# Performance work log

Hardware: AMD Instinct MI355X
Metric: run time of the kernel (lower is better)

The kernel has to match this reference:

```python
import jax, jax.numpy as jnp
import numpy as np

B, N, D, H = 8, 2048, 128, 8
HD = D // H  # head_depth = 16
CLIP = 10.0
INF = 1e10
THETA = 10000.0
SCALE_BASE = 512.0
LOGIT_SCALE = float(np.log(400.0) / np.log(50.0) / np.sqrt(HD))


def _rotate_half(x):
    # interleaved pairs: (x1, x2) -> (-x2, x1)
    x1 = x[..., ::2]
    x2 = x[..., 1::2]
    return jnp.stack((-x2, x1), axis=-1).reshape(x.shape)


def _rope_xpos(n, hd):
    # rotary_embedding_torch RotaryEmbedding(dim=hd, use_xpos=True)
    inv_freq = 1.0 / (THETA ** (jnp.arange(0, hd, 2, dtype=jnp.float32) / hd))  # (hd/2,)
    t = jnp.arange(n, dtype=jnp.float32)
    freqs = t[:, None] * inv_freq[None, :]          # (n, hd/2)
    freqs = jnp.repeat(freqs, 2, axis=-1)           # (n, hd) interleaved dup
    sc = (jnp.arange(0, hd, 2, dtype=jnp.float32) + 0.4 * hd) / (1.4 * hd)  # (hd/2,)
    power = (t - (n // 2)) / SCALE_BASE             # centered positions
    scale = sc[None, :] ** power[:, None]           # (n, hd/2)
    scale = jnp.repeat(scale, 2, axis=-1)           # (n, hd)
    return freqs, scale


def setup_inputs() -> dict:
    key = jax.random.key(0)
    ks = jax.random.split(key, 7)
    stdv_qkv = 1.0 / np.sqrt(HD)
    stdv_out = 1.0 / np.sqrt(D)
    q = jax.random.normal(ks[0], (B, N, D), dtype=jnp.float32)
    k = jax.random.normal(ks[1], (B, N, D), dtype=jnp.float32)
    v = jax.random.normal(ks[2], (B, N, D), dtype=jnp.float32)
    Wq = jax.random.uniform(ks[3], (D, D), minval=-stdv_qkv, maxval=stdv_qkv, dtype=jnp.float32)
    Wk = jax.random.uniform(ks[4], (D, D), minval=-stdv_qkv, maxval=stdv_qkv, dtype=jnp.float32)
    Wv = jax.random.uniform(ks[5], (D, D), minval=-stdv_qkv, maxval=stdv_qkv, dtype=jnp.float32)
    Wout = jax.random.uniform(ks[6], (D, D), minval=-stdv_out, maxval=stdv_out, dtype=jnp.float32)
    mask = jnp.zeros((B, N, 1), dtype=bool)
    return {"q": q, "k": k, "v": v, "Wq": Wq, "Wk": Wk, "Wv": Wv, "Wout": Wout, "mask": mask}


def reference(q, k, v, Wq, Wk, Wv, Wout, mask):
    def split_heads(t, W):
        # torch Linear (bias=False): t @ W.T, then (B,N,H,HD) -> (B,H,N,HD)
        return (t @ W.T).reshape(B, N, H, HD).transpose(0, 2, 1, 3)

    Qh = split_heads(q, Wq)
    Kh = split_heads(k, Wk)
    Vh = split_heads(v, Wv)

    freqs, scale = _rope_xpos(N, HD)  # (N, HD) each, broadcast over (B,H,N,HD)
    cos, sin = jnp.cos(freqs), jnp.sin(freqs)
    Qr = Qh * (cos * scale) + _rotate_half(Qh) * (sin * scale)
    inv_scale = 1.0 / scale
    Kr = Kh * (cos * inv_scale) + _rotate_half(Kh) * (sin * inv_scale)

    logits = jnp.einsum('bhqd,bhkd->bhqk', Qr, Kr) * LOGIT_SCALE
    logits = CLIP * jnp.tanh(logits)
    # mask: (B,N,1) bool, True -> masked; broadcast to (B,1,1,N)
    logits = jnp.where(mask[:, None, None, :, 0], -INF, logits)
    probs = jax.nn.softmax(logits, axis=-1)
    out = jnp.einsum('bhqk,bhkd->bhqd', probs, Vh)
    out = out.transpose(0, 2, 1, 3).reshape(B, N, D)
    return out @ Wout.T
```

## Files before the change

### kernel.cpp

```cpp
#include <hip/hip_runtime.h>
#include <math.h>

#define BB 8
#define NN 2048
#define DD 128
#define HH 8

typedef _Float16 v4h __attribute__((ext_vector_type(4)));
typedef float    v4f __attribute__((ext_vector_type(4)));
struct h8 { v4h a, b; };

__device__ __forceinline__ v4f zero4() { v4f z = {0.f, 0.f, 0.f, 0.f}; return z; }

__device__ __forceinline__ v4f mfma16(v4h a, v4h b, v4f c) {
    return __builtin_amdgcn_mfma_f32_16x16x16f16(a, b, c, 0, 0, 0);
}

__device__ __forceinline__ float fexp2(float x) {
#if __has_builtin(__builtin_amdgcn_exp2f)
    return __builtin_amdgcn_exp2f(x);
#else
    return __expf(x * 0.69314718055994531f);
#endif
}

#define QSCALE 1.10478088f
#define C1F 14.426950408889634f
#define C2F 28.853900817779268f

__global__ __launch_bounds__(256) void prep_kernel(
    const float* __restrict__ Wq, const float* __restrict__ Wk,
    const float* __restrict__ Wv, const float* __restrict__ Wo,
    _Float16* __restrict__ WH, _Float16* __restrict__ WoH,
    float* __restrict__ rtab)
{
    int tid = blockIdx.x * 256 + threadIdx.x;
    int m = tid >> 14, i = tid & 16383;
    const float* src = (m == 0) ? Wq : (m == 1) ? Wk : (m == 2) ? Wv : Wo;
    float wv = src[i];
    if (m < 3) WH[m * 16384 + i] = (_Float16)wv;
    else       WoH[i] = (_Float16)wv;

    if (tid < NN * 16) {
        int t = tid >> 4, hd = tid & 15, j = hd >> 1;
        const float invf_tab[8] = {1.f, 0.31622776601683794f, 0.1f, 0.031622776601683791f,
                                   0.01f, 0.0031622776601683794f, 0.001f, 0.00031622776601683794f};
        float freq = (float)t * invf_tab[j];
        float c = cosf(freq), s = sinf(freq);
        float scf = ((float)(2 * j) + 6.4f) / 22.4f;
        float pw  = ((float)t - 1024.0f) / 512.0f;
        float scl = exp2f(pw * log2f(scf));
        rtab[0 * NN * 16 + tid] = c * scl * QSCALE;
        rtab[1 * NN * 16 + tid] = s * scl * QSCALE;
        float is = 1.0f / scl;
        rtab[2 * NN * 16 + tid] = c * is;
        rtab[3 * NN * 16 + tid] = s * is;
    }
}

__global__ __launch_bounds__(256) void proj_rope_kernel(
    const float* __restrict__ q, const float* __restrict__ k, const float* __restrict__ v,
    const _Float16* __restrict__ WH, const float* __restrict__ rtab,
    _Float16* __restrict__ Qr, _Float16* __restrict__ Kr, _Float16* __restrict__ VT)
{
    __shared__ __align__(16) _Float16 xb[64][136];
    const int tid = threadIdx.x;
    const int m  = blockIdx.y;
    const int r0 = blockIdx.x * 64;
    const int b  = r0 >> 11;
    const int n0 = r0 & 2047;

    const float* s = ((m == 0) ? q : (m == 1) ? k : v) + (size_t)r0 * 128;
    #pragma unroll
    for (int i = 0; i < 8; ++i) {
        int u = tid + i * 256;
        int row = u >> 5, c4 = (u & 31) * 4;
        v4f f = *(const v4f*)(s + row * 128 + c4);
        v4h hv; hv[0]=(_Float16)f[0]; hv[1]=(_Float16)f[1]; hv[2]=(_Float16)f[2]; hv[3]=(_Float16)f[3];
        *(v4h*)&xb[row][c4] = hv;
    }
    __syncthreads();

    const int w = tid >> 6, lane = tid & 63;
    const int l16 = lane & 15, quad = lane >> 4;

    v4h xf[8];
    #pragma unroll
    for (int kt = 0; kt < 8; ++kt)
        xf[kt] = *(const v4h*)&xb[w * 16 + l16][kt * 16 + quad * 4];
    const _Float16* Wm = WH + m * 16384;
    v4f acc[8];
    #pragma unroll
    for (int ct = 0; ct < 8; ++ct) acc[ct] = zero4();
    #pragma unroll
    for (int kt = 0; kt < 8; ++kt) {
        #pragma unroll
        for (int ct = 0; ct < 8; ++ct) {
            v4h wf = *(const v4h*)(Wm + (ct * 16 + l16) * 128 + kt * 16 + quad * 4);
            if (m < 2) acc[ct] = mfma16(wf, xf[kt], acc[ct]);
            else       acc[ct] = mfma16(xf[kt], wf, acc[ct]);
        }
    }
    if (m < 2) {
        const float* tc = rtab + (m == 0 ? 0 : 2 * NN * 16);
        const float* ts = tc + NN * 16;
        const int n = n0 + w * 16 + l16;
        _Float16* dst = (m == 0 ? Qr : Kr);
        #pragma unroll
        for (int ct = 0; ct < 8; ++ct) {
            v4f cs = *(const v4f*)(tc + n * 16 + quad * 4);
            v4f sn = *(const v4f*)(ts + n * 16 + quad * 4);
            v4f a = acc[ct];
            v4f rot; rot[0] = -a[1]; rot[1] = a[0]; rot[2] = -a[3]; rot[3] = a[2];
            v4h o;
            #pragma unroll
            for (int r = 0; r < 4; ++r) o[r] = (_Float16)(a[r] * cs[r] + rot[r] * sn[r]);
            *(v4h*)(dst + ((size_t)(b * 8 + ct) * NN + n) * 16 + quad * 4) = o;
        }
    } else {
        #pragma unroll
        for (int ct = 0; ct < 8; ++ct) {
            v4f a = acc[ct];
            v4h o;
            #pragma unroll
            for (int r = 0; r < 4; ++r) o[r] = (_Float16)a[r];
            *(v4h*)(VT + ((size_t)(b * 8 + ct) * 16 + l16) * NN + n0 + w * 16 + quad * 4) = o;
        }
    }
}

__global__ __launch_bounds__(64) void attn_kernel(
    const _Float16* __restrict__ Qr, const _Float16* __restrict__ Kr,
    const _Float16* __restrict__ VT, const unsigned char* __restrict__ mask,
    _Float16* __restrict__ Obuf)
{
    __shared__ __align__(16) _Float16 Kt[2][64][20];
    __shared__ __align__(16) _Float16 VTt[2][16][68];
    __shared__ __align__(16) float    av[2][64];

    const int tid = threadIdx.x;
    const int bh = blockIdx.x >> 6;
    const int qt = blockIdx.x & 63;
    const int b = bh >> 3, h = bh & 7;
    const int q0 = qt * 32;
    const int l16 = tid & 15, quad = tid >> 4;

    const _Float16* Kbase = Kr + (size_t)bh * NN * 16;
    const _Float16* Vbase = VT + (size_t)bh * 16 * NN;
    const unsigned char* mbase = mask + b * NN;

    v4h qf[2];
    #pragma unroll
    for (int g = 0; g < 2; ++g)
        qf[g] = *(const v4h*)(Qr + ((size_t)bh * NN + q0 + g * 16 + l16) * 16 + quad * 4);

    v4f ot[2], sa[2];
    #pragma unroll
    for (int g = 0; g < 2; ++g) { ot[g] = zero4(); sa[g] = zero4(); }
    v4h ones; ones[0] = ones[1] = ones[2] = ones[3] = (_Float16)1.f;

    const int vrow = tid >> 2, vcol = (tid & 3) * 16;

    {
        h8 kA = *(const h8*)(Kbase + (size_t)tid * 16);
        h8 kB = *(const h8*)(Kbase + (size_t)tid * 16 + 8);
        h8 vA = *(const h8*)(Vbase + (size_t)vrow * NN + vcol);
        h8 vB = *(const h8*)(Vbase + (size_t)vrow * NN + vcol + 8);
        float a0 = mbase[tid] ? -1e30f : C1F;
        *(v4h*)&Kt[0][tid][0]  = kA.a;  *(v4h*)&Kt[0][tid][4]  = kA.b;
        *(v4h*)&Kt[0][tid][8]  = kB.a;  *(v4h*)&Kt[0][tid][12] = kB.b;
        *(v4h*)&VTt[0][vrow][vcol]      = vA.a;  *(v4h*)&VTt[0][vrow][vcol + 4]  = vA.b;
        *(v4h*)&VTt[0][vrow][vcol + 8]  = vB.a;  *(v4h*)&VTt[0][vrow][vcol + 12] = vB.b;
        av[0][tid] = a0;
    }

    for (int t = 0; t < 32; ++t) {
        const int cur = t & 1, nxt = cur ^ 1;
        const int nk = ((t + 1) & 31) * 64;

        h8 kA = *(const h8*)(Kbase + (size_t)(nk + tid) * 16);
        h8 kB = *(const h8*)(Kbase + (size_t)(nk + tid) * 16 + 8);
        h8 vA = *(const h8*)(Vbase + (size_t)vrow * NN + nk + vcol);
        h8 vB = *(const h8*)(Vbase + (size_t)vrow * NN + nk + vcol + 8);
        float an = mbase[nk + tid] ? -1e30f : C1F;

        #pragma unroll
        for (int st = 0; st < 4; ++st) {
            v4h kf = *(const v4h*)&Kt[cur][st * 16 + l16][quad * 4];
            v4f ad = *(const v4f*)&av[cur][st * 16 + quad * 4];
            v4h vf = *(const v4h*)&VTt[cur][l16][st * 16 + quad * 4];
            #pragma unroll
            for (int g = 0; g < 2; ++g) {
                v4f sv = mfma16(kf, qf[g], zero4());
                v4h ph;
                #pragma unroll
                for (int r = 0; r < 4; ++r) {
                    float u  = fexp2(sv[r]);
                    float rc = __builtin_amdgcn_rcpf(u + 1.f);
                    ph[r] = (_Float16)fexp2(__builtin_fmaf(rc, -C2F, ad[r]));
                }
                ot[g] = mfma16(vf, ph, ot[g]);
                sa[g] = mfma16(ones, ph, sa[g]);
            }
        }

        *(v4h*)&Kt[nxt][tid][0]  = kA.a;  *(v4h*)&Kt[nxt][tid][4]  = kA.b;
        *(v4h*)&Kt[nxt][tid][8]  = kB.a;  *(v4h*)&Kt[nxt][tid][12] = kB.b;
        *(v4h*)&VTt[nxt][vrow][vcol]      = vA.a;  *(v4h*)&VTt[nxt][vrow][vcol + 4]  = vA.b;
        *(v4h*)&VTt[nxt][vrow][vcol + 8]  = vB.a;  *(v4h*)&VTt[nxt][vrow][vcol + 12] = vB.b;
        av[nxt][tid] = an;
    }

    #pragma unroll
    for (int g = 0; g < 2; ++g) {
        float rd = 1.0f / sa[g][0];
        v4h o;
        #pragma unroll
        for (int r = 0; r < 4; ++r) o[r] = (_Float16)(ot[g][r] * rd);
        *(v4h*)(Obuf + ((size_t)(b * NN + q0 + g * 16 + l16) * 128) + h * 16 + quad * 4) = o;
    }
}

__global__ __launch_bounds__(256) void outproj_kernel(
    const _Float16* __restrict__ Obuf, const _Float16* __restrict__ WoH,
    float* __restrict__ out)
{
    __shared__ __align__(16) _Float16 ob[64][136];
    const int tid = threadIdx.x;
    const int r0 = blockIdx.x * 64;
    const int ct0 = blockIdx.y * 4;
    #pragma unroll
    for (int i = 0; i < 8; ++i) {
        int u = tid + i * 256;
        int row = u >> 5, c4 = (u & 31) * 4;
        *(v4h*)&ob[row][c4] = *(const v4h*)(Obuf + (size_t)(r0 + row) * 128 + c4);
    }
    __syncthreads();
    const int w = tid >> 6, lane = tid & 63;
    const int l16 = lane & 15, quad = lane >> 4;
    v4h af[8];
    #pragma unroll
    for (int kt = 0; kt < 8; ++kt)
        af[kt] = *(const v4h*)&ob[w * 16 + l16][kt * 16 + quad * 4];
    v4f acc[4];
    #pragma unroll
    for (int c = 0; c < 4; ++c) acc[c] = zero4();
    #pragma unroll
    for (int kt = 0; kt < 8; ++kt)
        #pragma unroll
        for (int c = 0; c < 4; ++c) {
            v4h wf = *(const v4h*)(WoH + ((ct0 + c) * 16 + l16) * 128 + kt * 16 + quad * 4);
            acc[c] = mfma16(af[kt], wf, acc[c]);
        }
    #pragma unroll
    for (int c = 0; c < 4; ++c)
        #pragma unroll
        for (int r = 0; r < 4; ++r)
            out[(size_t)(r0 + w * 16 + quad * 4 + r) * 128 + (ct0 + c) * 16 + l16] = acc[c][r];
}

extern "C" void kernel_launch(void* const* d_in, const int* in_sizes, int n_in,
                              void* d_out, int out_size, void* d_ws, size_t ws_size,
                              hipStream_t stream)
{
    const float* q  = (const float*)d_in[0];
    const float* k  = (const float*)d_in[1];
    const float* v  = (const float*)d_in[2];
    const float* Wq = (const float*)d_in[3];
    const float* Wk = (const float*)d_in[4];
    const float* Wv = (const float*)d_in[5];
    const float* Wo = (const float*)d_in[6];
    const unsigned char* mask = (const unsigned char*)d_in[7];
    float* out = (float*)d_out;

    char* ws = (char*)d_ws;
    _Float16* WH   = (_Float16*)(ws);
    _Float16* WoH  = (_Float16*)(ws + 98304);
    float*    rtab = (float*)(ws + 131072);
    _Float16* Qr   = (_Float16*)(ws + 655360);
    _Float16* Kr   = (_Float16*)(ws + 4849664);
    _Float16* VTd  = (_Float16*)(ws + 9043968);
    _Float16* Obuf = (_Float16*)(ws + 13238272);

    prep_kernel<<<256, 256, 0, stream>>>(Wq, Wk, Wv, Wo, WH, WoH, rtab);
    proj_rope_kernel<<<dim3(256, 3), 256, 0, stream>>>(q, k, v, WH, rtab, Qr, Kr, VTd);
    attn_kernel<<<4096, 64, 0, stream>>>(Qr, Kr, VTd, mask, Obuf);
    outproj_kernel<<<dim3(256, 2), 256, 0, stream>>>(Obuf, WoH, out);
}
```

Baseline: 211.6 us.

## Switch all matmuls to 16x16x32 f16 MFMA with LDS P re-layout

Replaces the 16x16x16 f16 MFMA with the wider 16x16x32 variant in the projection, attention and output-projection kernels. In attention, the QK^T product zero-pads K and Q to 32-deep, so the score MFMA does twice the nominal work. The probability tile is written to an LDS staging buffer and reread in the 8-wide B layout so PV and row-sum use half as many MFMAs over 32 keys. This adds LDS round-trips and padded compute in the hot loop in exchange for fewer MFMA issues. Only a wave-level reordering is relied on, with no explicit barrier around the P buffer.

```diff
diff --git a/kernel.cpp b/kernel.cpp
--- a/kernel.cpp
+++ b/kernel.cpp
@@ -7,13 +7,13 @@
 #define HH 8
 
 typedef _Float16 v4h __attribute__((ext_vector_type(4)));
+typedef _Float16 v8h __attribute__((ext_vector_type(8)));
 typedef float    v4f __attribute__((ext_vector_type(4)));
-struct h8 { v4h a, b; };
 
 __device__ __forceinline__ v4f zero4() { v4f z = {0.f, 0.f, 0.f, 0.f}; return z; }
 
-__device__ __forceinline__ v4f mfma16(v4h a, v4h b, v4f c) {
-    return __builtin_amdgcn_mfma_f32_16x16x16f16(a, b, c, 0, 0, 0);
+__device__ __forceinline__ v4f mfma32(v8h a, v8h b, v4f c) {
+    return __builtin_amdgcn_mfma_f32_16x16x32_f16(a, b, c, 0, 0, 0);
 }
 
 __device__ __forceinline__ float fexp2(float x) {
@@ -84,21 +84,21 @@
     const int w = tid >> 6, lane = tid & 63;
     const int l16 = lane & 15, quad = lane >> 4;
 
-    v4h xf[8];
-    #pragma unroll
-    for (int kt = 0; kt < 8; ++kt)
-        xf[kt] = *(const v4h*)&xb[w * 16 + l16][kt * 16 + quad * 4];
+    v8h xf[4];
+    #pragma unroll
+    for (int kt = 0; kt < 4; ++kt)
+        xf[kt] = *(const v8h*)&xb[w * 16 + l16][kt * 32 + quad * 8];
     const _Float16* Wm = WH + m * 16384;
     v4f acc[8];
     #pragma unroll
     for (int ct = 0; ct < 8; ++ct) acc[ct] = zero4();
     #pragma unroll
-    for (int kt = 0; kt < 8; ++kt) {
+    for (int kt = 0; kt < 4; ++kt) {
         #pragma unroll
         for (int ct = 0; ct < 8; ++ct) {
-            v4h wf = *(const v4h*)(Wm + (ct * 16 + l16) * 128 + kt * 16 + quad * 4);
-            if (m < 2) acc[ct] = mfma16(wf, xf[kt], acc[ct]);
-            else       acc[ct] = mfma16(xf[kt], wf, acc[ct]);
+            v8h wf = *(const v8h*)(Wm + (ct * 16 + l16) * 128 + kt * 32 + quad * 8);
+            if (m < 2) acc[ct] = mfma32(wf, xf[kt], acc[ct]);
+            else       acc[ct] = mfma32(xf[kt], wf, acc[ct]);
         }
     }
     if (m < 2) {
@@ -134,8 +134,9 @@
     const _Float16* __restrict__ VT, const unsigned char* __restrict__ mask,
     _Float16* __restrict__ Obuf)
 {
-    __shared__ __align__(16) _Float16 Kt[2][64][20];
-    __shared__ __align__(16) _Float16 VTt[2][16][68];
+    __shared__ __align__(16) _Float16 Kt[2][64][40];
+    __shared__ __align__(16) _Float16 VTt[2][16][72];
+    __shared__ __align__(16) _Float16 Pl[2][16][40];
     __shared__ __align__(16) float    av[2][64];
 
     const int tid = threadIdx.x;
@@ -149,28 +150,34 @@
     const _Float16* Vbase = VT + (size_t)bh * 16 * NN;
     const unsigned char* mbase = mask + b * NN;
 
-    v4h qf[2];
-    #pragma unroll
-    for (int g = 0; g < 2; ++g)
-        qf[g] = *(const v4h*)(Qr + ((size_t)bh * NN + q0 + g * 16 + l16) * 16 + quad * 4);
+    v8h z8 = {};
+    *(v8h*)&Kt[0][tid][16] = z8;  *(v8h*)&Kt[0][tid][24] = z8;
+    *(v8h*)&Kt[1][tid][16] = z8;  *(v8h*)&Kt[1][tid][24] = z8;
+
+    v8h qf8[2] = {z8, z8};
+    if (quad < 2) {
+        #pragma unroll
+        for (int g = 0; g < 2; ++g)
+            qf8[g] = *(const v8h*)(Qr + ((size_t)bh * NN + q0 + g * 16 + l16) * 16 + quad * 8);
+    }
 
     v4f ot[2], sa[2];
     #pragma unroll
     for (int g = 0; g < 2; ++g) { ot[g] = zero4(); sa[g] = zero4(); }
-    v4h ones; ones[0] = ones[1] = ones[2] = ones[3] = (_Float16)1.f;
+    v8h ones8;
+    #pragma unroll
+    for (int i = 0; i < 8; ++i) ones8[i] = (_Float16)1.f;
 
     const int vrow = tid >> 2, vcol = (tid & 3) * 16;
 
     {
-        h8 kA = *(const h8*)(Kbase + (size_t)tid * 16);
-        h8 kB = *(const h8*)(Kbase + (size_t)tid * 16 + 8);
-        h8 vA = *(const h8*)(Vbase + (size_t)vrow * NN + vcol);
-        h8 vB = *(const h8*)(Vbase + (size_t)vrow * NN + vcol + 8);
+        v8h kA = *(const v8h*)(Kbase + (size_t)tid * 16);
+        v8h kB = *(const v8h*)(Kbase + (size_t)tid * 16 + 8);
+        v8h vA = *(const v8h*)(Vbase + (size_t)vrow * NN + vcol);
+        v8h vB = *(const v8h*)(Vbase + (size_t)vrow * NN + vcol + 8);
         float a0 = mbase[tid] ? -1e30f : C1F;
-        *(v4h*)&Kt[0][tid][0]  = kA.a;  *(v4h*)&Kt[0][tid][4]  = kA.b;
-        *(v4h*)&Kt[0][tid][8]  = kB.a;  *(v4h*)&Kt[0][tid][12] = kB.b;
-        *(v4h*)&VTt[0][vrow][vcol]      = vA.a;  *(v4h*)&VTt[0][vrow][vcol + 4]  = vA.b;
-        *(v4h*)&VTt[0][vrow][vcol + 8]  = vB.a;  *(v4h*)&VTt[0][vrow][vcol + 12] = vB.b;
+        *(v8h*)&Kt[0][tid][0] = kA;  *(v8h*)&Kt[0][tid][8] = kB;
+        *(v8h*)&VTt[0][vrow][vcol] = vA;  *(v8h*)&VTt[0][vrow][vcol + 8] = vB;
         av[0][tid] = a0;
     }
 
@@ -178,36 +185,45 @@
         const int cur = t & 1, nxt = cur ^ 1;
         const int nk = ((t + 1) & 31) * 64;
 
-        h8 kA = *(const h8*)(Kbase + (size_t)(nk + tid) * 16);
-        h8 kB = *(const h8*)(Kbase + (size_t)(nk + tid) * 16 + 8);
-        h8 vA = *(const h8*)(Vbase + (size_t)vrow * NN + nk + vcol);
-        h8 vB = *(const h8*)(Vbase + (size_t)vrow * NN + nk + vcol + 8);
+        v8h kA = *(const v8h*)(Kbase + (size_t)(nk + tid) * 16);
+        v8h kB = *(const v8h*)(Kbase + (size_t)(nk + tid) * 16 + 8);
+        v8h vA = *(const v8h*)(Vbase + (size_t)vrow * NN + nk + vcol);
+        v8h vB = *(const v8h*)(Vbase + (size_t)vrow * NN + nk + vcol + 8);
         float an = mbase[nk + tid] ? -1e30f : C1F;
 
+        v8h kf8[4]; v4f ad4[4];
         #pragma unroll
         for (int st = 0; st < 4; ++st) {
-            v4h kf = *(const v4h*)&Kt[cur][st * 16 + l16][quad * 4];
-            v4f ad = *(const v4f*)&av[cur][st * 16 + quad * 4];
-            v4h vf = *(const v4h*)&VTt[cur][l16][st * 16 + quad * 4];
+            kf8[st] = *(const v8h*)&Kt[cur][st * 16 + l16][quad * 8];
+            ad4[st] = *(const v4f*)&av[cur][st * 16 + quad * 4];
+        }
+
+        #pragma unroll
+        for (int pair = 0; pair < 2; ++pair) {
+            v8h vf8 = *(const v8h*)&VTt[cur][l16][pair * 32 + quad * 8];
             #pragma unroll
             for (int g = 0; g < 2; ++g) {
-                v4f sv = mfma16(kf, qf[g], zero4());
-                v4h ph;
                 #pragma unroll
-                for (int r = 0; r < 4; ++r) {
-                    float u  = fexp2(sv[r]);
-                    float rc = __builtin_amdgcn_rcpf(u + 1.f);
-                    ph[r] = (_Float16)fexp2(__builtin_fmaf(rc, -C2F, ad[r]));
+                for (int stH = 0; stH < 2; ++stH) {
+                    const int st = pair * 2 + stH;
+                    v4f sv = mfma32(kf8[st], qf8[g], zero4());
+                    v4h ph;
+                    #pragma unroll
+                    for (int r = 0; r < 4; ++r) {
+                        float u  = fexp2(sv[r]);
+                        float rc = __builtin_amdgcn_rcpf(u + 1.f);
+                        ph[r] = (_Float16)fexp2(__builtin_fmaf(rc, -C2F, ad4[st][r]));
+                    }
+                    *(v4h*)&Pl[g][l16][stH * 16 + quad * 4] = ph;
                 }
-                ot[g] = mfma16(vf, ph, ot[g]);
-                sa[g] = mfma16(ones, ph, sa[g]);
+                v8h B8 = *(const v8h*)&Pl[g][l16][quad * 8];
+                ot[g] = mfma32(vf8, B8, ot[g]);
+                sa[g] = mfma32(ones8, B8, sa[g]);
             }
         }
 
-        *(v4h*)&Kt[nxt][tid][0]  = kA.a;  *(v4h*)&Kt[nxt][tid][4]  = kA.b;
-        *(v4h*)&Kt[nxt][tid][8]  = kB.a;  *(v4h*)&Kt[nxt][tid][12] = kB.b;
-        *(v4h*)&VTt[nxt][vrow][vcol]      = vA.a;  *(v4h*)&VTt[nxt][vrow][vcol + 4]  = vA.b;
-        *(v4h*)&VTt[nxt][vrow][vcol + 8]  = vB.a;  *(v4h*)&VTt[nxt][vrow][vcol + 12] = vB.b;
+        *(v8h*)&Kt[nxt][tid][0] = kA;  *(v8h*)&Kt[nxt][tid][8] = kB;
+        *(v8h*)&VTt[nxt][vrow][vcol] = vA;  *(v8h*)&VTt[nxt][vrow][vcol + 8] = vB;
         av[nxt][tid] = an;
     }
 
@@ -238,19 +254,19 @@
     __syncthreads();
     const int w = tid >> 6, lane = tid & 63;
     const int l16 = lane & 15, quad = lane >> 4;
-    v4h af[8];
-    #pragma unroll
-    for (int kt = 0; kt < 8; ++kt)
-        af[kt] = *(const v4h*)&ob[w * 16 + l16][kt * 16 + quad * 4];
+    v8h af[4];
+    #pragma unroll
+    for (int kt = 0; kt < 4; ++kt)
+        af[kt] = *(const v8h*)&ob[w * 16 + l16][kt * 32 + quad * 8];
     v4f acc[4];
     #pragma unroll
     for (int c = 0; c < 4; ++c) acc[c] = zero4();
     #pragma unroll
-    for (int kt = 0; kt < 8; ++kt)
+    for (int kt = 0; kt < 4; ++kt)
         #pragma unroll
         for (int c = 0; c < 4; ++c) {
-            v4h wf = *(const v4h*)(WoH + ((ct0 + c) * 16 + l16) * 128 + kt * 16 + quad * 4);
-            acc[c] = mfma16(af[kt], wf, acc[c]);
+            v8h wf = *(const v8h*)(WoH + ((ct0 + c) * 16 + l16) * 128 + kt * 32 + quad * 8);
+            acc[c] = mfma32(af[kt], wf, acc[c]);
         }
     #pragma unroll
     for (int c = 0; c < 4; ++c)
```

Measured after the change: 220.7 us. 4.3% more time.
